# Performance work log

Hardware: AMD Instinct MI355X
Metric: run time of the kernel (lower is better)

## Reference

```python
import jax, jax.numpy as jnp
import numpy as np

C = 256        # in_channels
HEADS = 8
HD = 64        # dim_heads
INNER = HEADS * HD   # 512
G = 32         # norm_groups
FF = 4 * INNER # 2048
EPS = 1e-5


def setup_inputs() -> dict:
    key = jax.random.key(0)
    ks = jax.random.split(key, 12)
    r = lambda k, shp: jax.random.normal(k, shp, jnp.float32) * 0.02
    return {
        "x": jax.random.normal(ks[0], (1, C, 16, 16, 16), jnp.float32),
        "gn_g": jnp.ones((C,), jnp.float32),
        "gn_b": jnp.zeros((C,), jnp.float32),
        "w_in": r(ks[1], (INNER, C)),   # Conv3d 1x1x1 as (out,in) matrix
        "b_in": jnp.zeros((INNER,), jnp.float32),
        "wq": r(ks[2], (INNER, INNER)),
        "wk": r(ks[3], (INNER, INNER)),
        "wv": r(ks[4], (INNER, INNER)),
        "ln1_g": jnp.ones((INNER,), jnp.float32),
        "ln1_b": jnp.zeros((INNER,), jnp.float32),
        "ff_w1": r(ks[5], (FF, INNER)),
        "ff_b1": jnp.zeros((FF,), jnp.float32),
        "ff_w2": r(ks[6], (INNER, FF)),
        "ff_b2": jnp.zeros((INNER,), jnp.float32),
        "ln2_g": jnp.ones((INNER,), jnp.float32),
        "ln2_b": jnp.zeros((INNER,), jnp.float32),
        "w_out": r(ks[7], (C, INNER)),  # Conv3d 1x1x1 back to C
        "b_out": jnp.zeros((C,), jnp.float32),
    }


def _group_norm(x, g, b):
    # x: (B,C,D,H,W), G groups, normalize over (C//G, D, H, W)
    B, Cc, D, H, W = x.shape
    xr = x.reshape(B, G, Cc // G, D, H, W)
    mu = jnp.mean(xr, axis=(2, 3, 4, 5), keepdims=True)
    var = jnp.var(xr, axis=(2, 3, 4, 5), keepdims=True)
    xr = (xr - mu) * jax.lax.rsqrt(var + EPS)
    xn = xr.reshape(B, Cc, D, H, W)
    return xn * g[None, :, None, None, None] + b[None, :, None, None, None]


def _layer_norm(x, g, b):
    mu = jnp.mean(x, axis=-1, keepdims=True)
    var = jnp.var(x, axis=-1, keepdims=True)
    return (x - mu) * jax.lax.rsqrt(var + EPS) * g + b


def reference(x, gn_g, gn_b, w_in, b_in, wq, wk, wv, ln1_g, ln1_b,
              ff_w1, ff_b1, ff_w2, ff_b2, ln2_g, ln2_b, w_out, b_out):
    B, Cc, D, H, W = x.shape
    x_in = x
    # GroupNorm + proj_in (1x1x1 conv == channel matmul)
    h = _group_norm(x, gn_g, gn_b)
    t = jnp.einsum('bcdhw,oc->bodhw', h, w_in) + b_in[None, :, None, None, None]
    N = D * H * W
    t = t.reshape(B, INNER, N).transpose(0, 2, 1)  # (B, N, INNER)

    # self-attention (manual einsum softmax einsum)
    q = (t @ wq.T).reshape(B, N, HEADS, HD)
    k = (t @ wk.T).reshape(B, N, HEADS, HD)
    v = (t @ wv.T).reshape(B, N, HEADS, HD)
    scale = HD ** (-0.5)
    scores = jnp.einsum('bihd,bjhd->bhij', q, k) * scale  # (B,H,N,N)
    attn = jax.nn.softmax(scores, axis=-1)
    o = jnp.einsum('bhij,bjhd->bihd', attn, v).reshape(B, N, INNER)
    # out_proj is Identity (q_dim == inner_dim), dropout=0
    t = _layer_norm(o + t, ln1_g, ln1_b)

    # FeedForward: Linear -> GELU (erf) -> Linear
    ff = jax.nn.gelu(t @ ff_w1.T + ff_b1, approximate=False) @ ff_w2.T + ff_b2
    t = _layer_norm(ff + t, ln2_g, ln2_b)

    # proj_out + residual
    y = t.transpose(0, 2, 1).reshape(B, INNER, D, H, W)
    out = jnp.einsum('bidhw,oi->bodhw', y, w_out) + b_out[None, :, None, None, None]
    return out + x_in
```

## Files before the change

### kernel.cpp

```cpp
#include <hip/hip_runtime.h>
#include <hip/hip_bf16.h>

typedef unsigned short u16;
typedef __attribute__((ext_vector_type(8))) short short8;
typedef __attribute__((ext_vector_type(4))) float floatx4;

#define LOG2E 1.44269504088896f
#define CEXP (0.125f * LOG2E)

static __device__ __forceinline__ u16 f2b(float f) {
  union { float f; unsigned u; } v; v.f = f;
  unsigned r = v.u + 0x7fffu + ((v.u >> 16) & 1u);
  return (u16)(r >> 16);
}
static __device__ __forceinline__ float b2f(u16 b) {
  union { float f; unsigned u; } v; v.u = ((unsigned)b) << 16;
  return v.f;
}
static __device__ __forceinline__ void async16(const u16* g, u16* l) {
  __builtin_amdgcn_global_load_lds(
      (const __attribute__((address_space(1))) unsigned int*)g,
      (__attribute__((address_space(3))) unsigned int*)l, 16, 0, 0);
}
static __device__ __forceinline__ float fexp2(float x) {
  return __builtin_amdgcn_exp2f(x);
}

__global__ __launch_bounds__(256) void f2b_all(
    const float* __restrict__ s0, const float* __restrict__ s1, const float* __restrict__ s2,
    const float* __restrict__ s3, const float* __restrict__ s4, const float* __restrict__ s5,
    const float* __restrict__ s6, const float* __restrict__ x,
    u16* __restrict__ d_win, u16* __restrict__ d_qkv, u16* __restrict__ d_f1,
    u16* __restrict__ d_f2, u16* __restrict__ d_wout, float2* __restrict__ cstats) {
  if (blockIdx.x >= 12288) {
    int c = blockIdx.x - 12288;
    const float4* p4 = (const float4*)(x + (size_t)c * 4096);
    float s = 0.f, ss = 0.f;
#pragma unroll
    for (int j = 0; j < 4; j++) {
      float4 v = p4[j * 256 + threadIdx.x];
      s += v.x + v.y + v.z + v.w;
      ss += v.x * v.x + v.y * v.y + v.z * v.z + v.w * v.w;
    }
    for (int m = 1; m < 64; m <<= 1) { s += __shfl_xor(s, m); ss += __shfl_xor(ss, m); }
    __shared__ float sb[8];
    int w = threadIdx.x >> 6;
    if ((threadIdx.x & 63) == 0) { sb[w * 2] = s; sb[w * 2 + 1] = ss; }
    __syncthreads();
    if (threadIdx.x == 0)
      cstats[c] = float2{sb[0] + sb[2] + sb[4] + sb[6], sb[1] + sb[3] + sb[5] + sb[7]};
    return;
  }
  int i = blockIdx.x * 256 + threadIdx.x;
  if (i < 131072) { d_win[i] = f2b(s0[i]); return; }
  i -= 131072;
  if (i < 262144) { d_qkv[i] = f2b(s1[i]); return; }
  i -= 262144;
  if (i < 262144) { d_qkv[262144 + i] = f2b(s2[i]); return; }
  i -= 262144;
  if (i < 262144) { d_qkv[524288 + i] = f2b(s3[i]); return; }
  i -= 262144;
  if (i < 1048576) { d_f1[i] = f2b(s4[i]); return; }
  i -= 1048576;
  if (i < 1048576) { d_f2[i] = f2b(s5[i]); return; }
  i -= 1048576;
  d_wout[i] = f2b(s6[i]);
}

__global__ __launch_bounds__(256) void gn_apply(const float* __restrict__ x, const float2* __restrict__ cstats,
                                                const float* __restrict__ gg, const float* __restrict__ gb,
                                                u16* __restrict__ hn) {
  int idx = blockIdx.x * 256 + threadIdx.x;
  int c = idx >> 12, n = idx & 4095;
  int g = c >> 3;
  float s = 0.f, ss = 0.f;
#pragma unroll
  for (int j = 0; j < 8; j++) {
    float2 p = cstats[g * 8 + j];
    s += p.x; ss += p.y;
  }
  float mu = s / 32768.f;
  float rs = rsqrtf(ss / 32768.f - mu * mu + 1e-5f);
  float v = (x[idx] - mu) * rs * gg[c] + gb[c];
  hn[(size_t)n * 256 + c] = f2b(v);
}

#define FLAG_BIAS 1
#define FLAG_GELU 2
#define FLAG_C16 8
#define FLAG_FINAL 32
#define FLAG_CZ 64

__global__ __launch_bounds__(256) void gemm_bt(
    const u16* __restrict__ A, const u16* __restrict__ B, const float* __restrict__ bias,
    float* __restrict__ C32, u16* __restrict__ C16, const float* __restrict__ resid,
    int M, int N, int K, int flags) {
  __shared__ u16 As[128 * 64];
  __shared__ u16 Bs[64 * 64];
  const int t = threadIdx.x;
  const int lane = t & 63;
  const int w = t >> 6;
  const int ln = lane & 15;
  const int quad = lane >> 4;
  const int m0 = blockIdx.x * 128;
  const int n0 = blockIdx.y * 64;
  const int wm = (w >> 1) * 64;
  const int wn = (w & 1) * 32;

  floatx4 acc[4][2];
#pragma unroll
  for (int i = 0; i < 4; i++)
#pragma unroll
    for (int j = 0; j < 2; j++) acc[i][j] = floatx4{0.f, 0.f, 0.f, 0.f};

  for (int k0 = 0; k0 < K; k0 += 64) {
    __syncthreads();
#pragma unroll
    for (int i = 0; i < 4; ++i) {
      int s = i * 256 + t;
      int row = s >> 3;
      int kb = (s & 7) ^ (row & 7);
      async16(A + (size_t)(m0 + row) * K + k0 + kb * 8, &As[(i * 256 + (t & ~63)) * 8]);
    }
#pragma unroll
    for (int i = 0; i < 2; ++i) {
      int s = i * 256 + t;
      int row = s >> 3;
      int kb = (s & 7) ^ (row & 7);
      async16(B + (size_t)(n0 + row) * K + k0 + kb * 8, &Bs[(i * 256 + (t & ~63)) * 8]);
    }
    __syncthreads();
#pragma unroll
    for (int ksi = 0; ksi < 2; ksi++) {
      short8 af[4], bfr[2];
      int kb = ksi * 4 + quad;
#pragma unroll
      for (int i = 0; i < 4; i++) {
        int m = wm + i * 16 + ln;
        af[i] = *(const short8*)&As[(m * 8 + (kb ^ (m & 7))) * 8];
      }
#pragma unroll
      for (int j = 0; j < 2; j++) {
        int n = wn + j * 16 + ln;
        bfr[j] = *(const short8*)&Bs[(n * 8 + (kb ^ (n & 7))) * 8];
      }
#pragma unroll
      for (int i = 0; i < 4; i++)
#pragma unroll
        for (int j = 0; j < 2; j++)
          acc[i][j] = __builtin_amdgcn_mfma_f32_16x16x32_bf16(af[i], bfr[j], acc[i][j], 0, 0, 0);
    }
  }

#pragma unroll
  for (int i = 0; i < 4; i++) {
#pragma unroll
    for (int j = 0; j < 2; j++) {
      int n = n0 + wn + j * 16 + ln;
      float bv = (flags & FLAG_BIAS) ? bias[n] : 0.f;
#pragma unroll
      for (int r = 0; r < 4; r++) {
        int m = m0 + wm + i * 16 + quad * 4 + r;
        float v = acc[i][j][r] + bv;
        if (flags & FLAG_C16) C16[(size_t)m * N + n] = f2b(v);
        if (flags & FLAG_FINAL)
          C32[(size_t)m * N + n] = v + bias[m] + resid[(size_t)m * N + n];
      }
    }
  }
}

__global__ __launch_bounds__(256) void gemm_big(
    const u16* __restrict__ A, const u16* __restrict__ B, const float* __restrict__ bias,
    u16* __restrict__ C16, int M, int N, int K, int flags) {
  __shared__ u16 As[128 * 64];
  __shared__ u16 Bs[128 * 64];
  const int t = threadIdx.x;
  const int lane = t & 63;
  const int w = t >> 6;
  const int ln = lane & 15;
  const int quad = lane >> 4;
  const int m0 = blockIdx.x * 128;
  const int n0 = blockIdx.y * 128;
  const int wm = (w >> 1) * 64;
  const int wn = (w & 1) * 64;
  const int kper = K / gridDim.z;
  const int kbeg = blockIdx.z * kper;

  floatx4 acc[4][4];
#pragma unroll
  for (int i = 0; i < 4; i++)
#pragma unroll
    for (int j = 0; j < 4; j++) acc[i][j] = floatx4{0.f, 0.f, 0.f, 0.f};

  for (int k0 = kbeg; k0 < kbeg + kper; k0 += 64) {
    __syncthreads();
#pragma unroll
    for (int i = 0; i < 4; ++i) {
      int s = i * 256 + t;
      int row = s >> 3;
      int kb = (s & 7) ^ (row & 7);
      async16(A + (size_t)(m0 + row) * K + k0 + kb * 8, &As[(i * 256 + (t & ~63)) * 8]);
      async16(B + (size_t)(n0 + row) * K + k0 + kb * 8, &Bs[(i * 256 + (t & ~63)) * 8]);
    }
    __syncthreads();
#pragma unroll
    for (int ksi = 0; ksi < 2; ksi++) {
      short8 af[4], bfr[4];
      int kb = ksi * 4 + quad;
#pragma unroll
      for (int i = 0; i < 4; i++) {
        int m = wm + i * 16 + ln;
        af[i] = *(const short8*)&As[(m * 8 + (kb ^ (m & 7))) * 8];
        int n = wn + i * 16 + ln;
        bfr[i] = *(const short8*)&Bs[(n * 8 + (kb ^ (n & 7))) * 8];
      }
#pragma unroll
      for (int i = 0; i < 4; i++)
#pragma unroll
        for (int j = 0; j < 4; j++)
          acc[i][j] = __builtin_amdgcn_mfma_f32_16x16x32_bf16(af[i], bfr[j], acc[i][j], 0, 0, 0);
    }
  }

  u16* Cdst = (flags & FLAG_CZ) ? C16 + (size_t)blockIdx.z * M * N : C16;
#pragma unroll
  for (int i = 0; i < 4; i++) {
#pragma unroll
    for (int j = 0; j < 4; j++) {
      int n = n0 + wn + j * 16 + ln;
      float bv = ((flags & FLAG_BIAS) && blockIdx.z == 0) ? bias[n] : 0.f;
#pragma unroll
      for (int r = 0; r < 4; r++) {
        int m = m0 + wm + i * 16 + quad * 4 + r;
        float v = acc[i][j][r] + bv;
        if (flags & FLAG_GELU) v = 0.5f * v * (1.f + erff(v * 0.70710678118f));
        Cdst[(size_t)m * N + n] = f2b(v);
      }
    }
  }
}

__global__ __launch_bounds__(256) void gemm_qkv(
    const u16* __restrict__ A, const u16* __restrict__ B,
    u16* __restrict__ Cq, u16* __restrict__ Ck, u16* __restrict__ CvT,
    int M, int K) {
  __shared__ u16 As[64 * 64];
  __shared__ u16 Bs[128 * 64];
  const int t = threadIdx.x;
  const int lane = t & 63;
  const int w = t >> 6;
  const int ln = lane & 15;
  const int quad = lane >> 4;
  const int m0 = blockIdx.x * 64;
  const int n0 = blockIdx.y * 128;
  const int wm = (w >> 1) * 32;
  const int wn = (w & 1) * 64;

  floatx4 acc[2][4];
#pragma unroll
  for (int i = 0; i < 2; i++)
#pragma unroll
    for (int j = 0; j < 4; j++) acc[i][j] = floatx4{0.f, 0.f, 0.f, 0.f};

  for (int k0 = 0; k0 < K; k0 += 64) {
    __syncthreads();
#pragma unroll
    for (int i = 0; i < 2; ++i) {
      int s = i * 256 + t;
      int row = s >> 3;
      int kb = (s & 7) ^ (row & 7);
      async16(A + (size_t)(m0 + row) * K + k0 + kb * 8, &As[(i * 256 + (t & ~63)) * 8]);
    }
#pragma unroll
    for (int i = 0; i < 4; ++i) {
      int s = i * 256 + t;
      int row = s >> 3;
      int kb = (s & 7) ^ (row & 7);
      async16(B + (size_t)(n0 + row) * K + k0 + kb * 8, &Bs[(i * 256 + (t & ~63)) * 8]);
    }
    __syncthreads();
#pragma unroll
    for (int ksi = 0; ksi < 2; ksi++) {
      short8 af[2], bfr[4];
      int kb = ksi * 4 + quad;
#pragma unroll
      for (int i = 0; i < 2; i++) {
        int m = wm + i * 16 + ln;
        af[i] = *(const short8*)&As[(m * 8 + (kb ^ (m & 7))) * 8];
      }
#pragma unroll
      for (int j = 0; j < 4; j++) {
        int n = wn + j * 16 + ln;
        bfr[j] = *(const short8*)&Bs[(n * 8 + (kb ^ (n & 7))) * 8];
      }
#pragma unroll
      for (int i = 0; i < 2; i++)
#pragma unroll
        for (int j = 0; j < 4; j++)
          acc[i][j] = __builtin_amdgcn_mfma_f32_16x16x32_bf16(af[i], bfr[j], acc[i][j], 0, 0, 0);
    }
  }

#pragma unroll
  for (int i = 0; i < 2; i++) {
#pragma unroll
    for (int j = 0; j < 4; j++) {
      int n = n0 + wn + j * 16 + ln;
#pragma unroll
      for (int r = 0; r < 4; r++) {
        int m = m0 + wm + i * 16 + quad * 4 + r;
        float v = acc[i][j][r];
        if (n < 512) Cq[(size_t)m * 512 + n] = f2b(v * CEXP);
        else if (n < 1024) Ck[(size_t)m * 512 + (n - 512)] = f2b(v);
        else CvT[(size_t)(n - 1024) * M + m] = f2b(v);
      }
    }
  }
}

__global__ __launch_bounds__(256, 4) void attn_kernel(
    const u16* __restrict__ Q, const u16* __restrict__ Km, const u16* __restrict__ VT,
    u16* __restrict__ Opart, float* __restrict__ ML, int Nseq, int kvLen) {
  __shared__ u16 Ks[2][64 * 64];
  __shared__ u16 Vs[2][64 * 64];
  __shared__ u16 Ps[4 * 32 * 64];
  const int t = threadIdx.x;
  const int lane = t & 63;
  const int w = t >> 6;
  const int ln = lane & 15;
  const int quad = lane >> 4;
  const int h = blockIdx.y;
  const int q0 = blockIdx.x * 128;
  const int split = blockIdx.z;
  const int kvbase = split * kvLen;
  u16* Opw = Opart + (size_t)split * Nseq * 512;
  u16* Pw = &Ps[w * 32 * 64];

  short8 qf[2][2];
#pragma unroll
  for (int qt = 0; qt < 2; qt++)
#pragma unroll
    for (int ksi = 0; ksi < 2; ksi++)
      qf[qt][ksi] = *(const short8*)&Q[(size_t)(q0 + w * 32 + qt * 16 + ln) * 512 + h * 64 + ksi * 32 + quad * 8];

  floatx4 accO[2][4];
#pragma unroll
  for (int qt = 0; qt < 2; qt++)
#pragma unroll
    for (int td = 0; td < 4; td++) accO[qt][td] = floatx4{0.f, 0.f, 0.f, 0.f};
  float lsum[2] = {0.f, 0.f};

  const int ntiles = kvLen >> 6;
#pragma unroll
  for (int i = 0; i < 2; ++i) {
    int s = i * 256 + t;
    int row = s >> 3;
    int kb = (s & 7) ^ (row & 7);
    async16(Km + (size_t)(kvbase + row) * 512 + h * 64 + kb * 8, &Ks[0][(i * 256 + (t & ~63)) * 8]);
    async16(VT + (size_t)(h * 64 + row) * Nseq + kvbase + kb * 8, &Vs[0][(i * 256 + (t & ~63)) * 8]);
  }

  for (int tile = 0; tile < ntiles; ++tile) {
    const int p = tile & 1;
    __syncthreads();
    if (tile + 1 < ntiles) {
      const int kv0 = kvbase + (tile + 1) * 64;
#pragma unroll
      for (int i = 0; i < 2; ++i) {
        int s = i * 256 + t;
        int row = s >> 3;
        int kb = (s & 7) ^ (row & 7);
        async16(Km + (size_t)(kv0 + row) * 512 + h * 64 + kb * 8, &Ks[p ^ 1][(i * 256 + (t & ~63)) * 8]);
        async16(VT + (size_t)(h * 64 + row) * Nseq + kv0 + kb * 8, &Vs[p ^ 1][(i * 256 + (t & ~63)) * 8]);
      }
    }
    const u16* Kc = Ks[p];
    const u16* Vc = Vs[p];

    floatx4 accS[2][4];
#pragma unroll
    for (int qt = 0; qt < 2; qt++)
#pragma unroll
      for (int tj = 0; tj < 4; tj++) accS[qt][tj] = floatx4{0.f, 0.f, 0.f, 0.f};
#pragma unroll
    for (int ksi = 0; ksi < 2; ksi++) {
      int kb = ksi * 4 + quad;
      short8 kf[4];
#pragma unroll
      for (int tj = 0; tj < 4; tj++) {
        int key = tj * 16 + ln;
        kf[tj] = *(const short8*)&Kc[(key * 8 + (kb ^ (key & 7))) * 8];
      }
#pragma unroll
      for (int qt = 0; qt < 2; qt++)
#pragma unroll
        for (int tj = 0; tj < 4; tj++)
          accS[qt][tj] = __builtin_amdgcn_mfma_f32_16x16x32_bf16(kf[tj], qf[qt][ksi], accS[qt][tj], 0, 0, 0);
    }

#pragma unroll
    for (int qt = 0; qt < 2; qt++) {
      int q8 = (qt * 16 + ln) * 8;
#pragma unroll
      for (int tj = 0; tj < 4; tj++) {
        float p0 = fexp2(accS[qt][tj][0]);
        float p1 = fexp2(accS[qt][tj][1]);
        float p2 = fexp2(accS[qt][tj][2]);
        float p3 = fexp2(accS[qt][tj][3]);
        lsum[qt] += (p0 + p1) + (p2 + p3);
        __hip_bfloat162 a01 = __float22bfloat162_rn(float2{p0, p1});
        __hip_bfloat162 a23 = __float22bfloat162_rn(float2{p2, p3});
        uint2 pk;
        pk.x = *(unsigned*)&a01;
        pk.y = *(unsigned*)&a23;
        int kbx = tj * 2 + (quad >> 1);
        *(uint2*)&Pw[(q8 + (kbx ^ (ln & 7))) * 8 + (quad & 1) * 4] = pk;
      }
    }

#pragma unroll
    for (int ksi = 0; ksi < 2; ksi++) {
      int kb = ksi * 4 + quad;
      short8 pf[2];
#pragma unroll
      for (int qt = 0; qt < 2; qt++)
        pf[qt] = *(const short8*)&Pw[((qt * 16 + ln) * 8 + (kb ^ (ln & 7))) * 8];
#pragma unroll
      for (int td = 0; td < 4; td++) {
        int d = td * 16 + ln;
        short8 vf = *(const short8*)&Vc[(d * 8 + (kb ^ (d & 7))) * 8];
#pragma unroll
        for (int qt = 0; qt < 2; qt++)
          accO[qt][td] = __builtin_amdgcn_mfma_f32_16x16x32_bf16(vf, pf[qt], accO[qt][td], 0, 0, 0);
      }
    }
  }

#pragma unroll
  for (int qt = 0; qt < 2; qt++) {
    lsum[qt] += __shfl_xor(lsum[qt], 16);
    lsum[qt] += __shfl_xor(lsum[qt], 32);
  }
#pragma unroll
  for (int qt = 0; qt < 2; qt++) {
    int q = q0 + w * 32 + qt * 16 + ln;
#pragma unroll
    for (int td = 0; td < 4; td++) {
      __hip_bfloat162 p01 = __float22bfloat162_rn(float2{accO[qt][td][0], accO[qt][td][1]});
      __hip_bfloat162 p23 = __float22bfloat162_rn(float2{accO[qt][td][2], accO[qt][td][3]});
      uint2 pk;
      pk.x = *(unsigned*)&p01;
      pk.y = *(unsigned*)&p23;
      *(uint2*)&Opw[(size_t)q * 512 + h * 64 + td * 16 + quad * 4] = pk;
    }
    if (quad == 0)
      ML[((size_t)split * 8 + h) * Nseq + q] = lsum[qt];
  }
}

__global__ __launch_bounds__(256) void ln_attn(
    const u16* __restrict__ Opart, const float* __restrict__ ML,
    const u16* __restrict__ t16, const float* __restrict__ g, const float* __restrict__ be,
    u16* __restrict__ o16) {
  int row = blockIdx.x;
  int t = threadIdx.x;
  size_t base = (size_t)row * 512;
  int c0 = 2 * t;
  int h = c0 >> 6;
  float lt = 0.f;
#pragma unroll
  for (int s = 0; s < 4; s++) lt += ML[((size_t)s * 8 + h) * 4096 + row];
  float a0 = 0.f, a1 = 0.f;
#pragma unroll
  for (int s = 0; s < 4; s++) {
    unsigned oo = *(const unsigned*)&Opart[(size_t)s * 4096 * 512 + base + c0];
    a0 += b2f((u16)(oo & 0xffff));
    a1 += b2f((u16)(oo >> 16));
  }
  unsigned tt = *(const unsigned*)&t16[base + c0];
  float inv = 1.0f / lt;
  float v0 = a0 * inv + b2f((u16)(tt & 0xffff));
  float v1 = a1 * inv + b2f((u16)(tt >> 16));
  float s = v0 + v1, ss = v0 * v0 + v1 * v1;
  for (int m = 1; m < 64; m <<= 1) { s += __shfl_xor(s, m); ss += __shfl_xor(ss, m); }
  __shared__ float sb[8];
  int w = t >> 6;
  if ((t & 63) == 0) { sb[w * 2] = s; sb[w * 2 + 1] = ss; }
  __syncthreads();
  s = sb[0] + sb[2] + sb[4] + sb[6];
  ss = sb[1] + sb[3] + sb[5] + sb[7];
  float mu = s / 512.f;
  float var = ss / 512.f - mu * mu;
  float rs = rsqrtf(var + 1e-5f);
  float2 gv = *(const float2*)&g[c0];
  float2 bv = *(const float2*)&be[c0];
  u16 r0 = f2b((v0 - mu) * rs * gv.x + bv.x);
  u16 r1 = f2b((v1 - mu) * rs * gv.y + bv.y);
  *(unsigned*)&o16[base + c0] = ((unsigned)r1 << 16) | r0;
}

__global__ __launch_bounds__(256) void ln_ff(
    const u16* __restrict__ zp, const u16* __restrict__ u,
    const float* __restrict__ g, const float* __restrict__ be, u16* __restrict__ o16) {
  int row = blockIdx.x;
  int t = threadIdx.x;
  size_t base = (size_t)row * 512;
  int c0 = 2 * t;
  unsigned uu = *(const unsigned*)&u[base + c0];
  float v0 = b2f((u16)(uu & 0xffff));
  float v1 = b2f((u16)(uu >> 16));
#pragma unroll
  for (int z = 0; z < 4; z++) {
    unsigned zz = *(const unsigned*)&zp[(size_t)z * 4096 * 512 + base + c0];
    v0 += b2f((u16)(zz & 0xffff));
    v1 += b2f((u16)(zz >> 16));
  }
  float s = v0 + v1, ss = v0 * v0 + v1 * v1;
  for (int m = 1; m < 64; m <<= 1) { s += __shfl_xor(s, m); ss += __shfl_xor(ss, m); }
  __shared__ float sb[8];
  int w = t >> 6;
  if ((t & 63) == 0) { sb[w * 2] = s; sb[w * 2 + 1] = ss; }
  __syncthreads();
  s = sb[0] + sb[2] + sb[4] + sb[6];
  ss = sb[1] + sb[3] + sb[5] + sb[7];
  float mu = s / 512.f;
  float var = ss / 512.f - mu * mu;
  float rs = rsqrtf(var + 1e-5f);
  float2 gv = *(const float2*)&g[c0];
  float2 bv = *(const float2*)&be[c0];
  u16 r0 = f2b((v0 - mu) * rs * gv.x + bv.x);
  u16 r1 = f2b((v1 - mu) * rs * gv.y + bv.y);
  *(unsigned*)&o16[base + c0] = ((unsigned)r1 << 16) | r0;
}

extern "C" void kernel_launch(void* const* d_in, const int* in_sizes, int n_in,
                              void* d_out, int out_size, void* d_ws, size_t ws_size,
                              hipStream_t stream) {
  const float* x = (const float*)d_in[0];
  const float* gn_g = (const float*)d_in[1];
  const float* gn_b = (const float*)d_in[2];
  const float* w_in = (const float*)d_in[3];
  const float* b_in = (const float*)d_in[4];
  const float* wq = (const float*)d_in[5];
  const float* wk = (const float*)d_in[6];
  const float* wv = (const float*)d_in[7];
  const float* ln1_g = (const float*)d_in[8];
  const float* ln1_b = (const float*)d_in[9];
  const float* ff_w1 = (const float*)d_in[10];
  const float* ff_b1 = (const float*)d_in[11];
  const float* ff_w2 = (const float*)d_in[12];
  const float* ff_b2 = (const float*)d_in[13];
  const float* ln2_g = (const float*)d_in[14];
  const float* ln2_b = (const float*)d_in[15];
  const float* w_out = (const float*)d_in[16];
  const float* b_out = (const float*)d_in[17];
  float* out = (float*)d_out;
  char* ws = (char*)d_ws;

  u16* w_in16 = (u16*)(ws + 0);
  u16* wqkv16 = (u16*)(ws + 262144);
  u16* fw116 = (u16*)(ws + 1835008);
  u16* fw216 = (u16*)(ws + 3932160);
  u16* wout16 = (u16*)(ws + 6029312);
  u16* u16b = (u16*)(ws + 6291456);
  u16* zp = (u16*)(ws + 10485760);
  u16* t16 = (u16*)(ws + 14680064);
  u16* qb = (u16*)(ws + 18874368);
  u16* kb = (u16*)(ws + 23068672);
  u16* vt = (u16*)(ws + 27262976);
  u16* zb = (u16*)(ws + 27262976);
  u16* opart = (u16*)(ws + 31457280);
  u16* g16 = (u16*)(ws + 31457280);
  float* ml = (float*)(ws + 48234496);
  u16* hn = (u16*)(ws + 49283072);
  float2* cstats = (float2*)(ws + 51380224);

  f2b_all<<<12544, 256, 0, stream>>>(w_in, wq, wk, wv, ff_w1, ff_w2, w_out, x,
                                     w_in16, wqkv16, fw116, fw216, wout16, cstats);
  gn_apply<<<4096, 256, 0, stream>>>(x, cstats, gn_g, gn_b, hn);

  gemm_bt<<<dim3(32, 8), 256, 0, stream>>>(hn, w_in16, b_in, nullptr, t16, nullptr,
                                           4096, 512, 256, FLAG_BIAS | FLAG_C16);
  gemm_qkv<<<dim3(64, 12), 256, 0, stream>>>(t16, wqkv16, qb, kb, vt, 4096, 512);
  attn_kernel<<<dim3(32, 8, 4), 256, 0, stream>>>(qb, kb, vt, opart, ml, 4096, 1024);
  ln_attn<<<4096, 256, 0, stream>>>(opart, ml, t16, ln1_g, ln1_b, u16b);
  gemm_big<<<dim3(32, 16), 256, 0, stream>>>(u16b, fw116, ff_b1, g16,
                                             4096, 2048, 512, FLAG_BIAS | FLAG_GELU | FLAG_C16);
  gemm_big<<<dim3(32, 4, 4), 256, 0, stream>>>(g16, fw216, ff_b2, zp,
                                               4096, 512, 2048, FLAG_BIAS | FLAG_CZ);
  ln_ff<<<4096, 256, 0, stream>>>(zp, u16b, ln2_g, ln2_b, zb);
  gemm_bt<<<dim3(2, 64), 256, 0, stream>>>(wout16, zb, b_out, out, nullptr, x,
                                           256, 4096, 512, FLAG_FINAL);
}
```

Measured before the change: 250.1 us.

## Transpose GroupNorm via LDS tile and shrink attention query tile without double buffering

GroupNorm apply now runs in 256 blocks of 16 positions each. Each block loads float4 rows into a padded LDS tile and writes coalesced channel-contiguous bf16 output, replacing the strided per-element scatter and per-thread stats recompute. The attention kernel drops from 32 to 16 queries per wave and from double-buffered to single-buffered K/V tiles, with two barriers per KV step, and the grid doubles. This lowers LDS and register use for higher occupancy. In exchange, loads no longer overlap compute, and each K/V tile is reused by half as many queries, doubling K/V traffic.

```diff
diff --git a/kernel.cpp b/kernel.cpp
--- a/kernel.cpp
+++ b/kernel.cpp
@@ -70,19 +70,35 @@
 __global__ __launch_bounds__(256) void gn_apply(const float* __restrict__ x, const float2* __restrict__ cstats,
                                                 const float* __restrict__ gg, const float* __restrict__ gb,
                                                 u16* __restrict__ hn) {
-  int idx = blockIdx.x * 256 + threadIdx.x;
-  int c = idx >> 12, n = idx & 4095;
-  int g = c >> 3;
-  float s = 0.f, ss = 0.f;
-#pragma unroll
-  for (int j = 0; j < 8; j++) {
-    float2 p = cstats[g * 8 + j];
-    s += p.x; ss += p.y;
-  }
-  float mu = s / 32768.f;
-  float rs = rsqrtf(ss / 32768.f - mu * mu + 1e-5f);
-  float v = (x[idx] - mu) * rs * gg[c] + gb[c];
-  hn[(size_t)n * 256 + c] = f2b(v);
+  __shared__ float tile[256 * 17];
+  __shared__ float gmu[32], grs[32];
+  int t = threadIdx.x;
+  if (t < 32) {
+    float s = 0.f, ss = 0.f;
+#pragma unroll
+    for (int j = 0; j < 8; j++) { float2 p = cstats[t * 8 + j]; s += p.x; ss += p.y; }
+    float mu = s / 32768.f;
+    gmu[t] = mu;
+    grs[t] = rsqrtf(ss / 32768.f - mu * mu + 1e-5f);
+  }
+  __syncthreads();
+  int n0 = blockIdx.x * 16;
+#pragma unroll
+  for (int j = 0; j < 4; j++) {
+    int c = j * 64 + (t >> 2);
+    int nl = (t & 3) * 4;
+    float4 v = *(const float4*)&x[(size_t)c * 4096 + n0 + nl];
+    float ga = gg[c] * grs[c >> 3];
+    float bb = gb[c] - gmu[c >> 3] * ga;
+    tile[c * 17 + nl + 0] = v.x * ga + bb;
+    tile[c * 17 + nl + 1] = v.y * ga + bb;
+    tile[c * 17 + nl + 2] = v.z * ga + bb;
+    tile[c * 17 + nl + 3] = v.w * ga + bb;
+  }
+  __syncthreads();
+#pragma unroll
+  for (int j = 0; j < 16; j++)
+    hn[(size_t)(n0 + j) * 256 + t] = f2b(tile[t * 17 + j]);
 }
 
 #define FLAG_BIAS 1
@@ -319,70 +335,51 @@
   }
 }
 
-__global__ __launch_bounds__(256, 4) void attn_kernel(
+__global__ __launch_bounds__(256) void attn_kernel(
     const u16* __restrict__ Q, const u16* __restrict__ Km, const u16* __restrict__ VT,
     u16* __restrict__ Opart, float* __restrict__ ML, int Nseq, int kvLen) {
-  __shared__ u16 Ks[2][64 * 64];
-  __shared__ u16 Vs[2][64 * 64];
-  __shared__ u16 Ps[4 * 32 * 64];
+  __shared__ u16 Ks[64 * 64];
+  __shared__ u16 Vs[64 * 64];
+  __shared__ u16 Ps[4 * 16 * 64];
   const int t = threadIdx.x;
   const int lane = t & 63;
   const int w = t >> 6;
   const int ln = lane & 15;
   const int quad = lane >> 4;
   const int h = blockIdx.y;
-  const int q0 = blockIdx.x * 128;
+  const int q0 = blockIdx.x * 64;
   const int split = blockIdx.z;
   const int kvbase = split * kvLen;
   u16* Opw = Opart + (size_t)split * Nseq * 512;
-  u16* Pw = &Ps[w * 32 * 64];
-
-  short8 qf[2][2];
-#pragma unroll
-  for (int qt = 0; qt < 2; qt++)
-#pragma unroll
-    for (int ksi = 0; ksi < 2; ksi++)
-      qf[qt][ksi] = *(const short8*)&Q[(size_t)(q0 + w * 32 + qt * 16 + ln) * 512 + h * 64 + ksi * 32 + quad * 8];
-
-  floatx4 accO[2][4];
-#pragma unroll
-  for (int qt = 0; qt < 2; qt++)
-#pragma unroll
-    for (int td = 0; td < 4; td++) accO[qt][td] = floatx4{0.f, 0.f, 0.f, 0.f};
-  float lsum[2] = {0.f, 0.f};
-
-  const int ntiles = kvLen >> 6;
-#pragma unroll
-  for (int i = 0; i < 2; ++i) {
-    int s = i * 256 + t;
-    int row = s >> 3;
-    int kb = (s & 7) ^ (row & 7);
-    async16(Km + (size_t)(kvbase + row) * 512 + h * 64 + kb * 8, &Ks[0][(i * 256 + (t & ~63)) * 8]);
-    async16(VT + (size_t)(h * 64 + row) * Nseq + kvbase + kb * 8, &Vs[0][(i * 256 + (t & ~63)) * 8]);
-  }
-
-  for (int tile = 0; tile < ntiles; ++tile) {
-    const int p = tile & 1;
-    __syncthreads();
-    if (tile + 1 < ntiles) {
-      const int kv0 = kvbase + (tile + 1) * 64;
-#pragma unroll
-      for (int i = 0; i < 2; ++i) {
-        int s = i * 256 + t;
-        int row = s >> 3;
-        int kb = (s & 7) ^ (row & 7);
-        async16(Km + (size_t)(kv0 + row) * 512 + h * 64 + kb * 8, &Ks[p ^ 1][(i * 256 + (t & ~63)) * 8]);
-        async16(VT + (size_t)(h * 64 + row) * Nseq + kv0 + kb * 8, &Vs[p ^ 1][(i * 256 + (t & ~63)) * 8]);
-      }
-    }
-    const u16* Kc = Ks[p];
-    const u16* Vc = Vs[p];
-
-    floatx4 accS[2][4];
-#pragma unroll
-    for (int qt = 0; qt < 2; qt++)
-#pragma unroll
-      for (int tj = 0; tj < 4; tj++) accS[qt][tj] = floatx4{0.f, 0.f, 0.f, 0.f};
+  u16* Pw = &Ps[w * 16 * 64];
+
+  short8 qf[2];
+#pragma unroll
+  for (int ksi = 0; ksi < 2; ksi++)
+    qf[ksi] = *(const short8*)&Q[(size_t)(q0 + w * 16 + ln) * 512 + h * 64 + ksi * 32 + quad * 8];
+
+  floatx4 accO[4];
+#pragma unroll
+  for (int td = 0; td < 4; td++) accO[td] = floatx4{0.f, 0.f, 0.f, 0.f};
+  float lsum = 0.f;
+  const int q8 = ln * 8;
+
+  for (int kv = 0; kv < kvLen; kv += 64) {
+    const int kv0 = kvbase + kv;
+    __syncthreads();
+#pragma unroll
+    for (int i = 0; i < 2; ++i) {
+      int s = i * 256 + t;
+      int row = s >> 3;
+      int kb = (s & 7) ^ (row & 7);
+      async16(Km + (size_t)(kv0 + row) * 512 + h * 64 + kb * 8, &Ks[(i * 256 + (t & ~63)) * 8]);
+      async16(VT + (size_t)(h * 64 + row) * Nseq + kv0 + kb * 8, &Vs[(i * 256 + (t & ~63)) * 8]);
+    }
+    __syncthreads();
+
+    floatx4 accS[4];
+#pragma unroll
+    for (int tj = 0; tj < 4; tj++) accS[tj] = floatx4{0.f, 0.f, 0.f, 0.f};
 #pragma unroll
     for (int ksi = 0; ksi < 2; ksi++) {
       int kb = ksi * 4 + quad;
@@ -390,73 +387,56 @@
 #pragma unroll
       for (int tj = 0; tj < 4; tj++) {
         int key = tj * 16 + ln;
-        kf[tj] = *(const short8*)&Kc[(key * 8 + (kb ^ (key & 7))) * 8];
-      }
-#pragma unroll
-      for (int qt = 0; qt < 2; qt++)
-#pragma unroll
-        for (int tj = 0; tj < 4; tj++)
-          accS[qt][tj] = __builtin_amdgcn_mfma_f32_16x16x32_bf16(kf[tj], qf[qt][ksi], accS[qt][tj], 0, 0, 0);
-    }
-
-#pragma unroll
-    for (int qt = 0; qt < 2; qt++) {
-      int q8 = (qt * 16 + ln) * 8;
-#pragma unroll
-      for (int tj = 0; tj < 4; tj++) {
-        float p0 = fexp2(accS[qt][tj][0]);
-        float p1 = fexp2(accS[qt][tj][1]);
-        float p2 = fexp2(accS[qt][tj][2]);
-        float p3 = fexp2(accS[qt][tj][3]);
-        lsum[qt] += (p0 + p1) + (p2 + p3);
-        __hip_bfloat162 a01 = __float22bfloat162_rn(float2{p0, p1});
-        __hip_bfloat162 a23 = __float22bfloat162_rn(float2{p2, p3});
-        uint2 pk;
-        pk.x = *(unsigned*)&a01;
-        pk.y = *(unsigned*)&a23;
-        int kbx = tj * 2 + (quad >> 1);
-        *(uint2*)&Pw[(q8 + (kbx ^ (ln & 7))) * 8 + (quad & 1) * 4] = pk;
-      }
+        kf[tj] = *(const short8*)&Ks[(key * 8 + (kb ^ (key & 7))) * 8];
+      }
+#pragma unroll
+      for (int tj = 0; tj < 4; tj++)
+        accS[tj] = __builtin_amdgcn_mfma_f32_16x16x32_bf16(kf[tj], qf[ksi], accS[tj], 0, 0, 0);
+    }
+
+#pragma unroll
+    for (int tj = 0; tj < 4; tj++) {
+      float p0 = fexp2(accS[tj][0]);
+      float p1 = fexp2(accS[tj][1]);
+      float p2 = fexp2(accS[tj][2]);
+      float p3 = fexp2(accS[tj][3]);
+      lsum += (p0 + p1) + (p2 + p3);
+      __hip_bfloat162 a01 = __float22bfloat162_rn(float2{p0, p1});
+      __hip_bfloat162 a23 = __float22bfloat162_rn(float2{p2, p3});
+      uint2 pk;
+      pk.x = *(unsigned*)&a01;
+      pk.y = *(unsigned*)&a23;
+      int kbx = tj * 2 + (quad >> 1);
+      *(uint2*)&Pw[(q8 + (kbx ^ (ln & 7))) * 8 + (quad & 1) * 4] = pk;
     }
 
 #pragma unroll
     for (int ksi = 0; ksi < 2; ksi++) {
       int kb = ksi * 4 + quad;
-      short8 pf[2];
-#pragma unroll
-      for (int qt = 0; qt < 2; qt++)
-        pf[qt] = *(const short8*)&Pw[((qt * 16 + ln) * 8 + (kb ^ (ln & 7))) * 8];
+      short8 pf = *(const short8*)&Pw[(q8 + (kb ^ (ln & 7))) * 8];
 #pragma unroll
       for (int td = 0; td < 4; td++) {
         int d = td * 16 + ln;
-        short8 vf = *(const short8*)&Vc[(d * 8 + (kb ^ (d & 7))) * 8];
-#pragma unroll
-        for (int qt = 0; qt < 2; qt++)
-          accO[qt][td] = __builtin_amdgcn_mfma_f32_16x16x32_bf16(vf, pf[qt], accO[qt][td], 0, 0, 0);
-      }
-    }
-  }
-
-#pragma unroll
-  for (int qt = 0; qt < 2; qt++) {
-    lsum[qt] += __shfl_xor(lsum[qt], 16);
-    lsum[qt] += __shfl_xor(lsum[qt], 32);
-  }
-#pragma unroll
-  for (int qt = 0; qt < 2; qt++) {
-    int q = q0 + w * 32 + qt * 16 + ln;
-#pragma unroll
-    for (int td = 0; td < 4; td++) {
-      __hip_bfloat162 p01 = __float22bfloat162_rn(float2{accO[qt][td][0], accO[qt][td][1]});
-      __hip_bfloat162 p23 = __float22bfloat162_rn(float2{accO[qt][td][2], accO[qt][td][3]});
-      uint2 pk;
-      pk.x = *(unsigned*)&p01;
-      pk.y = *(unsigned*)&p23;
-      *(uint2*)&Opw[(size_t)q * 512 + h * 64 + td * 16 + quad * 4] = pk;
-    }
-    if (quad == 0)
-      ML[((size_t)split * 8 + h) * Nseq + q] = lsum[qt];
-  }
+        short8 vf = *(const short8*)&Vs[(d * 8 + (kb ^ (d & 7))) * 8];
+        accO[td] = __builtin_amdgcn_mfma_f32_16x16x32_bf16(vf, pf, accO[td], 0, 0, 0);
+      }
+    }
+  }
+
+  lsum += __shfl_xor(lsum, 16);
+  lsum += __shfl_xor(lsum, 32);
+  int q = q0 + w * 16 + ln;
+#pragma unroll
+  for (int td = 0; td < 4; td++) {
+    __hip_bfloat162 p01 = __float22bfloat162_rn(float2{accO[td][0], accO[td][1]});
+    __hip_bfloat162 p23 = __float22bfloat162_rn(float2{accO[td][2], accO[td][3]});
+    uint2 pk;
+    pk.x = *(unsigned*)&p01;
+    pk.y = *(unsigned*)&p23;
+    *(uint2*)&Opw[(size_t)q * 512 + h * 64 + td * 16 + quad * 4] = pk;
+  }
+  if (quad == 0)
+    ML[((size_t)split * 8 + h) * Nseq + q] = lsum;
 }
 
 __global__ __launch_bounds__(256) void ln_attn(
@@ -578,12 +558,12 @@
 
   f2b_all<<<12544, 256, 0, stream>>>(w_in, wq, wk, wv, ff_w1, ff_w2, w_out, x,
                                      w_in16, wqkv16, fw116, fw216, wout16, cstats);
-  gn_apply<<<4096, 256, 0, stream>>>(x, cstats, gn_g, gn_b, hn);
+  gn_apply<<<256, 256, 0, stream>>>(x, cstats, gn_g, gn_b, hn);
 
   gemm_bt<<<dim3(32, 8), 256, 0, stream>>>(hn, w_in16, b_in, nullptr, t16, nullptr,
                                            4096, 512, 256, FLAG_BIAS | FLAG_C16);
   gemm_qkv<<<dim3(64, 12), 256, 0, stream>>>(t16, wqkv16, qb, kb, vt, 4096, 512);
-  attn_kernel<<<dim3(32, 8, 4), 256, 0, stream>>>(qb, kb, vt, opart, ml, 4096, 1024);
+  attn_kernel<<<dim3(64, 8, 4), 256, 0, stream>>>(qb, kb, vt, opart, ml, 4096, 1024);
   ln_attn<<<4096, 256, 0, stream>>>(opart, ml, t16, ln1_g, ln1_b, u16b);
   gemm_big<<<dim3(32, 16), 256, 0, stream>>>(u16b, fw116, ff_b1, g16,
                                              4096, 2048, 512, FLAG_BIAS | FLAG_GELU | FLAG_C16);
```

After: 253.8 us. Within noise of the previous version (+1.5%).
